# Kernel tuning notes

Hardware: AMD Instinct MI355X
Metric: run time of the kernel (lower is better)

## Reference

```python
import jax, jax.numpy as jnp
import numpy as np

EPS = 1e-05
B, M, N, P = 32, 1024, 1024, 256


def _xavier(key, shape):
    fan_in, fan_out = shape[0], shape[1]
    limit = np.sqrt(6.0 / (fan_in + fan_out))
    return jax.random.uniform(key, shape, jnp.float32, -limit, limit)


def setup_inputs() -> dict:
    key = jax.random.key(0)
    ks = jax.random.split(key, 6)
    return {
        "x": jax.random.normal(ks[0], (B, M, N), jnp.float32),
        "original_xj_y": _xavier(ks[1], (N, P)),
        "original_xi_y": _xavier(ks[2], (M, P)),
        "permuted_xj_y": _xavier(ks[3], (M, P)),
        "permuted_xi_y": _xavier(ks[4], (N, P)),
        "gamma_o_sum": jnp.ones((P,), jnp.float32),
        "gamma_o": jnp.ones((P, P), jnp.float32),
        "gamma_p_sum": jnp.ones((P,), jnp.float32),
        "gamma_p": jnp.ones((P, P), jnp.float32),
        "gamma": jnp.ones((P, P), jnp.float32),
        "beta_o_sum": jnp.zeros((P,), jnp.float32),
        "beta_o": jnp.zeros((P, P), jnp.float32),
        "beta_p_sum": jnp.zeros((P,), jnp.float32),
        "beta_p": jnp.zeros((P, P), jnp.float32),
        "beta": jnp.zeros((P, P), jnp.float32),
    }


def _normalize(x, axes, gamma, beta):
    mean = jnp.mean(x, axis=axes, keepdims=True)
    std = jnp.sqrt(jnp.var(x, axis=axes, keepdims=True, ddof=1))  # torch std is unbiased
    return gamma * ((x - mean) / (std + EPS)) + beta


def reference(x, original_xj_y, original_xi_y, permuted_xj_y, permuted_xi_y,
              gamma_o_sum, gamma_o, gamma_p_sum, gamma_p, gamma,
              beta_o_sum, beta_o, beta_p_sum, beta_p, beta):
    permuted = jnp.swapaxes(x, -1, -2)  # [B, N, M]

    # original path
    oyy = x @ original_xj_y                      # [B, M, P]
    o_sum = _normalize(oyy.sum(axis=-2), (-1,), gamma_o_sum, beta_o_sum) + 1.0  # [B, P]
    oyy = jnp.swapaxes(oyy, -1, -2) @ original_xi_y  # [B, P, P]
    oyy = jnp.swapaxes(oyy, -1, -2)
    oyy = _normalize(oyy, (-2, -1), gamma_o, beta_o)

    # permuted path
    pyy = permuted @ permuted_xj_y               # [B, N, P]
    p_sum = _normalize(pyy.sum(axis=-2), (-1,), gamma_p_sum, beta_p_sum) + 1.0  # [B, P]
    pyy = jnp.swapaxes(pyy, -1, -2) @ permuted_xi_y  # [B, P, P]
    pyy = jnp.swapaxes(pyy, -1, -2)
    pyy = _normalize(pyy, (-2, -1), gamma_p, beta_p)

    relations = jnp.einsum('ij,ik->ijk', o_sum, p_sum)  # [B, P, P]
    projected = (oyy * relations) @ (pyy * relations)   # [B, P, P]
    projected = _normalize(projected, (-2, -1), gamma, beta)
    return (projected, relations)
```

## Files before the change

kernel.cpp:

```cpp
#include <hip/hip_runtime.h>
#include <hip/hip_bf16.h>

#define PP 256
#define BB 32
#define MM 1024
#define NN 1024

constexpr float EPSF = 1e-5f;

typedef __attribute__((ext_vector_type(8))) short short8v;
typedef __attribute__((ext_vector_type(4))) short short4v;
typedef __attribute__((ext_vector_type(4))) float f32x4;

__device__ inline float bf2f(short s) {
  union { unsigned u; float f; } cv;
  cv.u = ((unsigned)(unsigned short)s) << 16;
  return cv.f;
}
__device__ inline short f2bf(float f) {
  union { float f; unsigned u; } cv; cv.f = f;
  unsigned u = cv.u;
  unsigned r = (u + 0x7fffu + ((u >> 16) & 1u)) >> 16;
  return (short)r;
}

__device__ inline void gload16(const void* g, void* l) {
  __builtin_amdgcn_global_load_lds(
      (const __attribute__((address_space(1))) unsigned*)g,
      (__attribute__((address_space(3))) unsigned*)l, 16, 0, 0);
}

__global__ __launch_bounds__(256)
void wconv4(const float* __restrict__ s0, const float* __restrict__ s1,
            const float* __restrict__ s2, const float* __restrict__ s3,
            short* __restrict__ d0, short* __restrict__ d1,
            short* __restrict__ d2, short* __restrict__ d3)
{
  const float* src = (blockIdx.z == 0) ? s0 : (blockIdx.z == 1) ? s1
                    : (blockIdx.z == 2) ? s2 : s3;
  short* dst = (blockIdx.z == 0) ? d0 : (blockIdx.z == 1) ? d1
              : (blockIdx.z == 2) ? d2 : d3;
  __shared__ float tile[64][65];
  const int c0 = blockIdx.x * 64, r0 = blockIdx.y * 64;
  const int tid = threadIdx.x;
#pragma unroll
  for (int i = 0; i < 16; ++i) {
    int idx = i * 256 + tid;
    int r = idx >> 6, c = idx & 63;
    tile[r][c] = src[(long)(r0 + r) * 256 + (c0 + c)];
  }
  __syncthreads();
#pragma unroll
  for (int i = 0; i < 16; ++i) {
    int idx = i * 256 + tid;
    int rr = idx >> 6, cc = idx & 63;
    dst[(long)(c0 + rr) * 1024 + (r0 + cc)] = f2bf(tile[cc][rr]);
  }
}

__global__ __launch_bounds__(256)
void tr2_f32(const float* __restrict__ s0, const float* __restrict__ s1,
             float* __restrict__ d0, float* __restrict__ d1)
{
  const float* src = blockIdx.z ? s1 : s0;
  float* dst = blockIdx.z ? d1 : d0;
  __shared__ float tile[64][65];
  const int c0 = blockIdx.x * 64, r0 = blockIdx.y * 64;
  const int tid = threadIdx.x;
#pragma unroll
  for (int i = 0; i < 16; ++i) {
    int idx = i * 256 + tid;
    int r = idx >> 6, c = idx & 63;
    tile[r][c] = src[(long)(r0 + r) * 256 + (c0 + c)];
  }
  __syncthreads();
#pragma unroll
  for (int i = 0; i < 16; ++i) {
    int idx = i * 256 + tid;
    int rr = idx >> 6, cc = idx & 63;
    dst[(long)(c0 + rr) * 256 + (r0 + cc)] = tile[cc][rr];
  }
}

__global__ __launch_bounds__(256, 4)
void gemm_xcat(const float* __restrict__ x, const short* __restrict__ wcat,
               short* __restrict__ oyyT, short* __restrict__ UT,
               float* __restrict__ rowsum)
{
  constexpr int BM = 128, BN = 128;
  __shared__ short As[2][4 * BM * 8];
  __shared__ short Bs[2][4 * BN * 8];

  const int b = blockIdx.z;
  const float* Ab = x + (long)b * MM * NN;
  const int m0 = blockIdx.x * BM;
  const int n0 = blockIdx.y * BN;

  const int tid = threadIdx.x;
  const int l = tid & 63, w = tid >> 6;
  const int wr = w >> 1, wc = w & 1;
  const int lk = l >> 4, lr = l & 15;
  const int sm = tid >> 2, skc = tid & 3;

  const float* aptr0 = Ab + (long)(m0 + sm) * NN + skc * 8;
  const float* aptr1 = Ab + (long)(m0 + 64 + sm) * NN + skc * 8;
  const int bn = tid & 127, bk0 = (tid >> 7) * 8;
  const short* bptr = wcat + (long)(n0 + bn) * NN + bk0;

  const int sA0 = ((skc * BM + sm) * 8) ^ (skc << 4);
  const int sA1 = ((skc * BM + 64 + sm) * 8) ^ (skc << 4);

  f32x4 acc[4][4];
#pragma unroll
  for (int fm = 0; fm < 4; ++fm)
#pragma unroll
    for (int fn = 0; fn < 4; ++fn)
      acc[fm][fn] = (f32x4){0.f, 0.f, 0.f, 0.f};

  float rs0 = 0.f, rs1 = 0.f;
  const bool doRs = (blockIdx.y == 0);
  float4 a00, a01, a10, a11;

#define XCAT_LOAD_A(k0_) do { \
    a00 = *reinterpret_cast<const float4*>(aptr0 + (k0_)); \
    a01 = *reinterpret_cast<const float4*>(aptr0 + (k0_) + 4); \
    a10 = *reinterpret_cast<const float4*>(aptr1 + (k0_)); \
    a11 = *reinterpret_cast<const float4*>(aptr1 + (k0_) + 4); \
  } while (0)

#define XCAT_STAGE_B(buf_, k0_) do { \
    gload16(bptr + (k0_), &Bs[buf_][tid * 8]); \
    gload16(bptr + (k0_) + 16, &Bs[buf_][(tid + 256) * 8]); \
  } while (0)

#define XCAT_STAGE_A(buf_) do { \
    if (doRs) { \
      rs0 += a00.x + a00.y + a00.z + a00.w + a01.x + a01.y + a01.z + a01.w; \
      rs1 += a10.x + a10.y + a10.z + a10.w + a11.x + a11.y + a11.z + a11.w; \
    } \
    short8v pk0, pk1; \
    pk0[0] = f2bf(a00.x); pk0[1] = f2bf(a00.y); pk0[2] = f2bf(a00.z); pk0[3] = f2bf(a00.w); \
    pk0[4] = f2bf(a01.x); pk0[5] = f2bf(a01.y); pk0[6] = f2bf(a01.z); pk0[7] = f2bf(a01.w); \
    pk1[0] = f2bf(a10.x); pk1[1] = f2bf(a10.y); pk1[2] = f2bf(a10.z); pk1[3] = f2bf(a10.w); \
    pk1[4] = f2bf(a11.x); pk1[5] = f2bf(a11.y); pk1[6] = f2bf(a11.z); pk1[7] = f2bf(a11.w); \
    *reinterpret_cast<short8v*>(&As[buf_][sA0]) = pk0; \
    *reinterpret_cast<short8v*>(&As[buf_][sA1]) = pk1; \
  } while (0)

  XCAT_LOAD_A(0);
  XCAT_STAGE_B(0, 0);
  XCAT_STAGE_A(0);
  __syncthreads();

  for (int kt = 0; kt < 32; ++kt) {
    const int cur = kt & 1, nxt = cur ^ 1;
    if (kt < 31) {
      const int k1 = (kt + 1) * 32;
      XCAT_LOAD_A(k1);
      XCAT_STAGE_B(nxt, k1);
    }
    short8v af[4], bf[4];
#pragma unroll
    for (int fm = 0; fm < 4; ++fm) {
      const int row = wr * 64 + fm * 16 + lr;
      af[fm] = *reinterpret_cast<const short8v*>(&As[cur][((lk * BM + row) * 8) ^ (lk << 4)]);
    }
#pragma unroll
    for (int fn = 0; fn < 4; ++fn)
      bf[fn] = *reinterpret_cast<const short8v*>(&Bs[cur][(lk * BN + wc * 64 + fn * 16 + lr) * 8]);
#pragma unroll
    for (int fm = 0; fm < 4; ++fm)
#pragma unroll
      for (int fn = 0; fn < 4; ++fn)
        acc[fm][fn] = __builtin_amdgcn_mfma_f32_16x16x32_bf16(
            af[fm], bf[fn], acc[fm][fn], 0, 0, 0);
    if (kt < 31) XCAT_STAGE_A(nxt);
    __syncthreads();
  }

  if (doRs) {
    rs0 += __shfl_xor(rs0, 1); rs0 += __shfl_xor(rs0, 2);
    rs1 += __shfl_xor(rs1, 1); rs1 += __shfl_xor(rs1, 2);
    if ((tid & 3) == 0) {
      rowsum[(long)b * MM + m0 + sm] = rs0;
      rowsum[(long)b * MM + m0 + 64 + sm] = rs1;
    }
  }

  short* Cb = ((n0 < 256) ? oyyT : UT) + (long)b * PP * MM;
  const int nb = n0 & 255;
#pragma unroll
  for (int fm = 0; fm < 4; ++fm)
#pragma unroll
    for (int fn = 0; fn < 4; ++fn) {
      const int c = nb + wc * 64 + fn * 16 + lr;
      const int rb = m0 + wr * 64 + fm * 16 + lk * 4;
      short4v pk;
#pragma unroll
      for (int j = 0; j < 4; ++j) pk[j] = f2bf(acc[fm][fn][j]);
      *reinterpret_cast<short4v*>(&Cb[(long)c * MM + rb]) = pk;
    }
}

__global__ __launch_bounds__(256)
void gemm_dual(const short* __restrict__ oyyT, const short* __restrict__ wo2T,
               const short* __restrict__ UT, const short* __restrict__ wp1T,
               float* __restrict__ t2T, float* __restrict__ p2)
{
  constexpr int BM = 64, BN = 64;
  __shared__ short As[2][4 * BM * 8];
  __shared__ short Bs[2][4 * BN * 8];

  const int z = blockIdx.z;
  const short* Ab; const short* Bb; float* Cb;
  if (z < 32) { Ab = oyyT + (long)z * PP * MM; Bb = wo2T; Cb = t2T + ((long)z << 16); }
  else { Ab = UT + (long)(z - 32) * PP * MM; Bb = wp1T; Cb = p2 + ((long)(z - 32) << 16); }

  const int m0 = blockIdx.x * BM, n0 = blockIdx.y * BN;
  const int tid = threadIdx.x;
  const int l = tid & 63, w = tid >> 6;
  const int wr = w >> 1, wc = w & 1;
  const int lk = l >> 4, lr = l & 15;
  const int kc = tid >> 6, mloc = tid & 63;
  const short* aP = Ab + (long)(m0 + mloc) * MM + kc * 8;
  const short* bP = Bb + (long)(n0 + mloc) * MM + kc * 8;

  f32x4 acc[2][2];
#pragma unroll
  for (int fm = 0; fm < 2; ++fm)
#pragma unroll
    for (int fn = 0; fn < 2; ++fn)
      acc[fm][fn] = (f32x4){0.f, 0.f, 0.f, 0.f};

  gload16(aP, &As[0][tid * 8]);
  gload16(bP, &Bs[0][tid * 8]);
  __syncthreads();

  for (int kt = 0; kt < 32; ++kt) {
    const int cur = kt & 1, nxt = cur ^ 1;
    if (kt < 31) {
      gload16(aP + (kt + 1) * 32, &As[nxt][tid * 8]);
      gload16(bP + (kt + 1) * 32, &Bs[nxt][tid * 8]);
    }
    short8v af[2], bf[2];
#pragma unroll
    for (int fm = 0; fm < 2; ++fm)
      af[fm] = *(const short8v*)&As[cur][(lk * BM + wr * 32 + fm * 16 + lr) * 8];
#pragma unroll
    for (int fn = 0; fn < 2; ++fn)
      bf[fn] = *(const short8v*)&Bs[cur][(lk * BN + wc * 32 + fn * 16 + lr) * 8];
#pragma unroll
    for (int fm = 0; fm < 2; ++fm)
#pragma unroll
      for (int fn = 0; fn < 2; ++fn)
        acc[fm][fn] = __builtin_amdgcn_mfma_f32_16x16x32_bf16(
            af[fm], bf[fn], acc[fm][fn], 0, 0, 0);
    __syncthreads();
  }

#pragma unroll
  for (int fm = 0; fm < 2; ++fm)
#pragma unroll
    for (int fn = 0; fn < 2; ++fn) {
      const int c = n0 + wc * 32 + fn * 16 + lr;
      const int rb = m0 + wr * 32 + fm * 16 + lk * 4;
      *(f32x4*)&Cb[(long)c * PP + rb] = acc[fm][fn];
    }
}

__global__ __launch_bounds__(256)
void gemm_pp(const short* __restrict__ A, const short* __restrict__ BT,
             float* __restrict__ C)
{
  constexpr int BM = 64, BN = 64;
  __shared__ short As[2][4 * BM * 8];
  __shared__ short Bs[2][4 * BN * 8];
  const int b = blockIdx.z;
  const short* Ab = A + ((long)b << 16);
  const short* Bb = BT + ((long)b << 16);
  float* Cb = C + ((long)b << 16);
  const int m0 = blockIdx.x * BM, n0 = blockIdx.y * BN;
  const int tid = threadIdx.x;
  const int l = tid & 63, w = tid >> 6;
  const int wr = w >> 1, wc = w & 1;
  const int lk = l >> 4, lr = l & 15;
  const int kc = tid >> 6, mloc = tid & 63;
  const short* aP = Ab + (long)(m0 + mloc) * PP + kc * 8;
  const short* bP = Bb + (long)(n0 + mloc) * PP + kc * 8;

  f32x4 acc[2][2];
#pragma unroll
  for (int fm = 0; fm < 2; ++fm)
#pragma unroll
    for (int fn = 0; fn < 2; ++fn)
      acc[fm][fn] = (f32x4){0.f, 0.f, 0.f, 0.f};

  gload16(aP, &As[0][tid * 8]);
  gload16(bP, &Bs[0][tid * 8]);
  __syncthreads();

  for (int kt = 0; kt < 8; ++kt) {
    const int cur = kt & 1, nxt = cur ^ 1;
    if (kt < 7) {
      gload16(aP + (kt + 1) * 32, &As[nxt][tid * 8]);
      gload16(bP + (kt + 1) * 32, &Bs[nxt][tid * 8]);
    }
    short8v af[2], bf[2];
#pragma unroll
    for (int fm = 0; fm < 2; ++fm)
      af[fm] = *(const short8v*)&As[cur][(lk * BM + wr * 32 + fm * 16 + lr) * 8];
#pragma unroll
    for (int fn = 0; fn < 2; ++fn)
      bf[fn] = *(const short8v*)&Bs[cur][(lk * BN + wc * 32 + fn * 16 + lr) * 8];
#pragma unroll
    for (int fm = 0; fm < 2; ++fm)
#pragma unroll
      for (int fn = 0; fn < 2; ++fn)
        acc[fm][fn] = __builtin_amdgcn_mfma_f32_16x16x32_bf16(
            af[fm], bf[fn], acc[fm][fn], 0, 0, 0);
    __syncthreads();
  }

#pragma unroll
  for (int fm = 0; fm < 2; ++fm)
#pragma unroll
    for (int fn = 0; fn < 2; ++fn) {
      const int c = n0 + wc * 32 + fn * 16 + lr;
      const int rb = m0 + wr * 32 + fm * 16 + lk * 4;
#pragma unroll
      for (int j = 0; j < 4; ++j)
        Cb[(long)(rb + j) * PP + c] = acc[fm][fn][j];
    }
}

__global__ __launch_bounds__(256)
void colsum_bf16(const short* __restrict__ srcT, float* __restrict__ raw)
{
  const int b = blockIdx.y;
  const int w = threadIdx.x >> 6, l = threadIdx.x & 63;
  const int p = blockIdx.x * 4 + w;
  const short* row = srcT + ((long)b * 256 + p) * 1024;
  short8v v1 = *(const short8v*)&row[l * 8];
  short8v v2 = *(const short8v*)&row[(64 + l) * 8];
  float s = 0.f;
#pragma unroll
  for (int j = 0; j < 8; ++j) s += bf2f(v1[j]) + bf2f(v2[j]);
#pragma unroll
  for (int off = 32; off; off >>= 1) s += __shfl_down(s, off);
  if (l == 0) raw[(long)b * 256 + p] = s;
}

__global__ __launch_bounds__(256)
void psum_dot(const short* __restrict__ wp1T, const float* __restrict__ rowsum,
              float* __restrict__ rawP)
{
  __shared__ float rsm[1024];
  const int b = blockIdx.x;
  for (int i = threadIdx.x; i < 1024; i += 256) rsm[i] = rowsum[(long)b * 1024 + i];
  __syncthreads();
  const int p = threadIdx.x;
  const short* wrow = wp1T + (long)p * 1024;
  float s = 0.f;
  for (int k = 0; k < 1024; k += 8) {
    short8v v = *(const short8v*)&wrow[k];
#pragma unroll
    for (int j = 0; j < 8; ++j) s = fmaf(bf2f(v[j]), rsm[k + j], s);
  }
  rawP[(long)b * 256 + p] = s;
}

__device__ inline void block_reduce2(float& v1, float& v2, float* red)
{
#pragma unroll
  for (int off = 32; off > 0; off >>= 1) {
    v1 += __shfl_down(v1, off);
    v2 += __shfl_down(v2, off);
  }
  const int lane = threadIdx.x & 63, wid = threadIdx.x >> 6;
  if (lane == 0) { red[wid * 2] = v1; red[wid * 2 + 1] = v2; }
  __syncthreads();
  v1 = red[0] + red[2] + red[4] + red[6];
  v2 = red[1] + red[3] + red[5] + red[7];
}

__global__ __launch_bounds__(256)
void norm_sum2(const float* __restrict__ raw2,
               const float* __restrict__ g_os, const float* __restrict__ b_os,
               const float* __restrict__ g_ps, const float* __restrict__ b_ps,
               float* __restrict__ o_sum, float* __restrict__ p_sum)
{
  const int bb = blockIdx.x;
  const bool isP = bb >= 32;
  const int b = bb & 31;
  const float* raw = raw2 + (isP ? 8192 : 0);
  const float* gamma = isP ? g_ps : g_os;
  const float* beta = isP ? b_ps : b_os;
  float* outp = isP ? p_sum : o_sum;
  const int p = threadIdx.x;
  float s = raw[(long)b * 256 + p];
  __shared__ float red[8];
  float v1 = s, v2 = s * s;
  block_reduce2(v1, v2, red);
  const float mean = v1 / 256.0f;
  float var = fmaxf((v2 - v1 * mean) / 255.0f, 0.f);
  const float inv = 1.0f / (sqrtf(var) + EPSF);
  outp[(long)b * 256 + p] = gamma[p] * (s - mean) * inv + beta[p] + 1.0f;
}

__global__ __launch_bounds__(256)
void stats_dual(const float* __restrict__ t2T, const float* __restrict__ p2,
                float* __restrict__ part)
{
  const int y = blockIdx.y, chunk = blockIdx.x;
  const float* s = (y < 32 ? t2T + ((long)y << 16)
                           : p2 + ((long)(y - 32) << 16)) + (long)chunk * 8192;
  float v1 = 0.f, v2 = 0.f;
  for (int i = threadIdx.x; i < 2048; i += 256) {
    float4 xv = *reinterpret_cast<const float4*>(&s[i * 4]);
    v1 += xv.x + xv.y + xv.z + xv.w;
    v2 = fmaf(xv.x, xv.x, fmaf(xv.y, xv.y, fmaf(xv.z, xv.z, fmaf(xv.w, xv.w, v2))));
  }
  __shared__ float red[8];
  block_reduce2(v1, v2, red);
  if (threadIdx.x == 0) {
    part[(y * 8 + chunk) * 2] = v1;
    part[(y * 8 + chunk) * 2 + 1] = v2;
  }
}

__global__ void stats_fin2(const float* __restrict__ part,
                           float* __restrict__ stO, float* __restrict__ stP)
{
  const int t = threadIdx.x;
  float v1 = 0.f, v2 = 0.f;
#pragma unroll
  for (int c = 0; c < 8; ++c) {
    v1 += part[(t * 8 + c) * 2];
    v2 += part[(t * 8 + c) * 2 + 1];
  }
  const float mean = v1 / 65536.0f;
  const float var = fmaxf((v2 - v1 * mean) / 65535.0f, 0.f);
  float* st = (t < 32) ? stO : stP;
  st[(t & 31) * 2] = mean;
  st[(t & 31) * 2 + 1] = 1.0f / (sqrtf(var) + EPSF);
}

__global__ __launch_bounds__(256)
void stats_part(const float* __restrict__ src, float* __restrict__ part)
{
  const int b = blockIdx.y, chunk = blockIdx.x;
  const float* s = src + ((long)b << 16) + (long)chunk * 8192;
  float v1 = 0.f, v2 = 0.f;
  for (int i = threadIdx.x; i < 2048; i += 256) {
    float4 xv = *reinterpret_cast<const float4*>(&s[i * 4]);
    v1 += xv.x + xv.y + xv.z + xv.w;
    v2 = fmaf(xv.x, xv.x, fmaf(xv.y, xv.y, fmaf(xv.z, xv.z, fmaf(xv.w, xv.w, v2))));
  }
  __shared__ float red[8];
  block_reduce2(v1, v2, red);
  if (threadIdx.x == 0) {
    part[(b * 8 + chunk) * 2] = v1;
    part[(b * 8 + chunk) * 2 + 1] = v2;
  }
}

__global__ void stats_fin(const float* __restrict__ part, float* __restrict__ st)
{
  const int b = threadIdx.x;
  if (b < 32) {
    float v1 = 0.f, v2 = 0.f;
#pragma unroll
    for (int c = 0; c < 8; ++c) {
      v1 += part[(b * 8 + c) * 2];
      v2 += part[(b * 8 + c) * 2 + 1];
    }
    const float mean = v1 / 65536.0f;
    const float var = fmaxf((v2 - v1 * mean) / 65535.0f, 0.f);
    st[b * 2] = mean;
    st[b * 2 + 1] = 1.0f / (sqrtf(var) + EPSF);
  }
}

__global__ __launch_bounds__(256)
void prep2(const float* __restrict__ t2T, const float* __restrict__ p2,
           const float* __restrict__ o_sum, const float* __restrict__ p_sum,
           const float* __restrict__ gamma_o, const float* __restrict__ beta_o,
           const float* __restrict__ gTp, const float* __restrict__ bTp,
           const float* __restrict__ stO, const float* __restrict__ stP,
           short* __restrict__ Ap, short* __restrict__ BpT,
           float* __restrict__ out)
{
  const long idx = (long)blockIdx.x * 256 + threadIdx.x;
  const int b = (int)(idx >> 16);
  const int rc = (int)(idx & 65535);
  const int r = rc >> 8, c = rc & 255;
  const float mO = stO[b * 2], iO = stO[b * 2 + 1];
  const float mP = stP[b * 2], iP = stP[b * 2 + 1];
  const float relA = o_sum[(b << 8) + r] * p_sum[(b << 8) + c];
  const float on = gamma_o[rc] * (t2T[idx] - mO) * iO + beta_o[rc];
  Ap[idx] = f2bf(on * relA);
  const float pn = gTp[rc] * (p2[idx] - mP) * iP + bTp[rc];
  BpT[idx] = f2bf(pn * o_sum[(b << 8) + c] * p_sum[(b << 8) + r]);
  out[(long)BB * 65536 + idx] = relA;
}

__global__ __launch_bounds__(256)
void final_half(const float* __restrict__ proj, const float* __restrict__ stF,
                const float* __restrict__ gamma, const float* __restrict__ beta,
                float* __restrict__ out)
{
  const long idx = (long)blockIdx.x * 256 + threadIdx.x;
  const int b = (int)(idx >> 16);
  const int ij = (int)(idx & 65535);
  out[idx] = gamma[ij] * (proj[idx] - stF[b * 2]) * stF[b * 2 + 1] + beta[ij];
}

extern "C" void kernel_launch(void* const* d_in, const int* in_sizes, int n_in,
                              void* d_out, int out_size, void* d_ws, size_t ws_size,
                              hipStream_t stream)
{
  const float* x    = (const float*)d_in[0];
  const float* Wo1  = (const float*)d_in[1];
  const float* Wo2  = (const float*)d_in[2];
  const float* Wp1  = (const float*)d_in[3];
  const float* Wp2  = (const float*)d_in[4];
  const float* g_os = (const float*)d_in[5];
  const float* g_o  = (const float*)d_in[6];
  const float* g_ps = (const float*)d_in[7];
  const float* g_p  = (const float*)d_in[8];
  const float* g    = (const float*)d_in[9];
  const float* b_os = (const float*)d_in[10];
  const float* b_o  = (const float*)d_in[11];
  const float* b_ps = (const float*)d_in[12];
  const float* b_p  = (const float*)d_in[13];
  const float* b_   = (const float*)d_in[14];
  float* out = (float*)d_out;

  short* wcat = (short*)d_ws;
  short* wo2T = wcat + 524288;
  short* wp1T = wo2T + 262144;
  short* oyyT = wp1T + 262144;
  short* UT   = oyyT + 8388608;
  float* gTp  = (float*)(UT + 8388608);
  float* bTp  = gTp + 65536;
  float* rowsumX = bTp + 65536;
  float* t2T  = rowsumX + 32768;
  float* p2   = t2T + 2097152;
  float* proj = p2 + 2097152;
  short* Ap   = (short*)(proj + 2097152);
  short* BpT  = Ap + 2097152;
  float* raw2 = (float*)(BpT + 2097152);
  float* o_sum = raw2 + 16384;
  float* p_sum = o_sum + 8192;
  float* part  = p_sum + 8192;
  float* partF = part + 1024;
  float* stO   = partF + 512;
  float* stP   = stO + 64;
  float* stF   = stP + 64;

  wconv4<<<dim3(4, 16, 4), 256, 0, stream>>>(Wo1, Wo2, Wp1, Wp2,
                                             wcat, wo2T, wp1T, wcat + 262144);
  tr2_f32<<<dim3(4, 4, 2), 256, 0, stream>>>(g_p, b_p, gTp, bTp);

  gemm_xcat<<<dim3(8, 4, 32), 256, 0, stream>>>(x, wcat, oyyT, UT, rowsumX);

  colsum_bf16<<<dim3(64, 32), 256, 0, stream>>>(oyyT, raw2);
  psum_dot<<<32, 256, 0, stream>>>(wp1T, rowsumX, raw2 + 8192);
  norm_sum2<<<64, 256, 0, stream>>>(raw2, g_os, b_os, g_ps, b_ps, o_sum, p_sum);

  gemm_dual<<<dim3(4, 4, 64), 256, 0, stream>>>(oyyT, wo2T, UT, wp1T, t2T, p2);

  stats_dual<<<dim3(8, 64), 256, 0, stream>>>(t2T, p2, part);
  stats_fin2<<<1, 64, 0, stream>>>(part, stO, stP);

  prep2<<<8192, 256, 0, stream>>>(t2T, p2, o_sum, p_sum, g_o, b_o, gTp, bTp,
                                  stO, stP, Ap, BpT, out);

  gemm_pp<<<dim3(4, 4, 32), 256, 0, stream>>>(Ap, BpT, proj);

  stats_part<<<dim3(8, 32), 256, 0, stream>>>(proj, partF);
  stats_fin<<<1, 64, 0, stream>>>(partF, stF);

  final_half<<<8192, 256, 0, stream>>>(proj, stF, g, b_, out);
}
```

Measured before the change: 168.9 us.

## Retile x GEMM to full-width 64x512 blocks and enlarge dual GEMM tiles

The first GEMM now uses 512-thread blocks that each cover 64 rows of x against all 512 output columns. Each x tile is therefore read from global memory and converted to bf16 only once, where before it was re-read by four column blocks. Half the threads load and convert A while the other half stage B, so the work is split between warps. The second GEMM grows its tiles from 64x64 to 128x128 for more reuse per block, at the cost of fewer blocks (256) and more registers and LDS per block.

```diff
diff --git a/kernel.cpp b/kernel.cpp
--- a/kernel.cpp
+++ b/kernel.cpp
@@ -82,33 +82,26 @@
   }
 }
 
-__global__ __launch_bounds__(256, 4)
+__global__ __launch_bounds__(512, 4)
 void gemm_xcat(const float* __restrict__ x, const short* __restrict__ wcat,
                short* __restrict__ oyyT, short* __restrict__ UT,
                float* __restrict__ rowsum)
 {
-  constexpr int BM = 128, BN = 128;
-  __shared__ short As[2][4 * BM * 8];
-  __shared__ short Bs[2][4 * BN * 8];
+  __shared__ short As[2][4 * 64 * 8];
+  __shared__ short Bs[2][4 * 512 * 8];
 
   const int b = blockIdx.z;
   const float* Ab = x + (long)b * MM * NN;
-  const int m0 = blockIdx.x * BM;
-  const int n0 = blockIdx.y * BN;
+  const int m0 = blockIdx.x * 64;
 
   const int tid = threadIdx.x;
   const int l = tid & 63, w = tid >> 6;
-  const int wr = w >> 1, wc = w & 1;
   const int lk = l >> 4, lr = l & 15;
-  const int sm = tid >> 2, skc = tid & 3;
-
-  const float* aptr0 = Ab + (long)(m0 + sm) * NN + skc * 8;
-  const float* aptr1 = Ab + (long)(m0 + 64 + sm) * NN + skc * 8;
-  const int bn = tid & 127, bk0 = (tid >> 7) * 8;
-  const short* bptr = wcat + (long)(n0 + bn) * NN + bk0;
-
-  const int sA0 = ((skc * BM + sm) * 8) ^ (skc << 4);
-  const int sA1 = ((skc * BM + 64 + sm) * 8) ^ (skc << 4);
+
+  const int sm = (tid >> 2) & 63, skc = tid & 3;
+  const float* aptr = Ab + (long)(m0 + sm) * NN + skc * 8;
+  const int sA = ((skc * 64 + sm) * 8) ^ (skc << 4);
+  const int t2 = tid & 255;
 
   f32x4 acc[4][4];
 #pragma unroll
@@ -117,84 +110,76 @@
     for (int fn = 0; fn < 4; ++fn)
       acc[fm][fn] = (f32x4){0.f, 0.f, 0.f, 0.f};
 
-  float rs0 = 0.f, rs1 = 0.f;
-  const bool doRs = (blockIdx.y == 0);
-  float4 a00, a01, a10, a11;
-
-#define XCAT_LOAD_A(k0_) do { \
-    a00 = *reinterpret_cast<const float4*>(aptr0 + (k0_)); \
-    a01 = *reinterpret_cast<const float4*>(aptr0 + (k0_) + 4); \
-    a10 = *reinterpret_cast<const float4*>(aptr1 + (k0_)); \
-    a11 = *reinterpret_cast<const float4*>(aptr1 + (k0_) + 4); \
+  float rs = 0.f;
+  float4 a0, a1;
+
+#define XC_LOAD_A(k0_) do { \
+    a0 = *reinterpret_cast<const float4*>(aptr + (k0_)); \
+    a1 = *reinterpret_cast<const float4*>(aptr + (k0_) + 4); \
   } while (0)
 
-#define XCAT_STAGE_B(buf_, k0_) do { \
-    gload16(bptr + (k0_), &Bs[buf_][tid * 8]); \
-    gload16(bptr + (k0_) + 16, &Bs[buf_][(tid + 256) * 8]); \
+#define XC_STAGE_B(buf_, k0_) do { \
+    _Pragma("unroll") \
+    for (int i = 0; i < 8; ++i) { \
+      const int n_ = ((i & 1) << 8) + t2; \
+      const int kc_ = i >> 1; \
+      gload16(wcat + (long)n_ * NN + (k0_) + kc_ * 8, \
+              &Bs[buf_][(kc_ * 512 + n_) * 8]); \
+    } \
   } while (0)
 
-#define XCAT_STAGE_A(buf_) do { \
-    if (doRs) { \
-      rs0 += a00.x + a00.y + a00.z + a00.w + a01.x + a01.y + a01.z + a01.w; \
-      rs1 += a10.x + a10.y + a10.z + a10.w + a11.x + a11.y + a11.z + a11.w; \
-    } \
-    short8v pk0, pk1; \
-    pk0[0] = f2bf(a00.x); pk0[1] = f2bf(a00.y); pk0[2] = f2bf(a00.z); pk0[3] = f2bf(a00.w); \
-    pk0[4] = f2bf(a01.x); pk0[5] = f2bf(a01.y); pk0[6] = f2bf(a01.z); pk0[7] = f2bf(a01.w); \
-    pk1[0] = f2bf(a10.x); pk1[1] = f2bf(a10.y); pk1[2] = f2bf(a10.z); pk1[3] = f2bf(a10.w); \
-    pk1[4] = f2bf(a11.x); pk1[5] = f2bf(a11.y); pk1[6] = f2bf(a11.z); pk1[7] = f2bf(a11.w); \
-    *reinterpret_cast<short8v*>(&As[buf_][sA0]) = pk0; \
-    *reinterpret_cast<short8v*>(&As[buf_][sA1]) = pk1; \
+#define XC_STAGE_A(buf_) do { \
+    rs += a0.x + a0.y + a0.z + a0.w + a1.x + a1.y + a1.z + a1.w; \
+    short8v pk; \
+    pk[0] = f2bf(a0.x); pk[1] = f2bf(a0.y); pk[2] = f2bf(a0.z); pk[3] = f2bf(a0.w); \
+    pk[4] = f2bf(a1.x); pk[5] = f2bf(a1.y); pk[6] = f2bf(a1.z); pk[7] = f2bf(a1.w); \
+    *reinterpret_cast<short8v*>(&As[buf_][sA]) = pk; \
   } while (0)
 
-  XCAT_LOAD_A(0);
-  XCAT_STAGE_B(0, 0);
-  XCAT_STAGE_A(0);
+  if (tid < 256) { XC_LOAD_A(0); XC_STAGE_A(0); }
+  else           { XC_STAGE_B(0, 0); }
   __syncthreads();
 
   for (int kt = 0; kt < 32; ++kt) {
     const int cur = kt & 1, nxt = cur ^ 1;
     if (kt < 31) {
       const int k1 = (kt + 1) * 32;
-      XCAT_LOAD_A(k1);
-      XCAT_STAGE_B(nxt, k1);
+      if (tid < 256) XC_LOAD_A(k1);
+      else           XC_STAGE_B(nxt, k1);
     }
     short8v af[4], bf[4];
 #pragma unroll
-    for (int fm = 0; fm < 4; ++fm) {
-      const int row = wr * 64 + fm * 16 + lr;
-      af[fm] = *reinterpret_cast<const short8v*>(&As[cur][((lk * BM + row) * 8) ^ (lk << 4)]);
-    }
+    for (int fm = 0; fm < 4; ++fm)
+      af[fm] = *reinterpret_cast<const short8v*>(
+          &As[cur][((lk * 64 + fm * 16 + lr) * 8) ^ (lk << 4)]);
 #pragma unroll
     for (int fn = 0; fn < 4; ++fn)
-      bf[fn] = *reinterpret_cast<const short8v*>(&Bs[cur][(lk * BN + wc * 64 + fn * 16 + lr) * 8]);
+      bf[fn] = *reinterpret_cast<const short8v*>(
+          &Bs[cur][(lk * 512 + w * 64 + fn * 16 + lr) * 8]);
 #pragma unroll
     for (int fm = 0; fm < 4; ++fm)
 #pragma unroll
       for (int fn = 0; fn < 4; ++fn)
         acc[fm][fn] = __builtin_amdgcn_mfma_f32_16x16x32_bf16(
             af[fm], bf[fn], acc[fm][fn], 0, 0, 0);
-    if (kt < 31) XCAT_STAGE_A(nxt);
+    if (kt < 31 && tid < 256) XC_STAGE_A(nxt);
     __syncthreads();
   }
 
-  if (doRs) {
-    rs0 += __shfl_xor(rs0, 1); rs0 += __shfl_xor(rs0, 2);
-    rs1 += __shfl_xor(rs1, 1); rs1 += __shfl_xor(rs1, 2);
-    if ((tid & 3) == 0) {
-      rowsum[(long)b * MM + m0 + sm] = rs0;
-      rowsum[(long)b * MM + m0 + 64 + sm] = rs1;
-    }
-  }
-
-  short* Cb = ((n0 < 256) ? oyyT : UT) + (long)b * PP * MM;
-  const int nb = n0 & 255;
+  if (tid < 256) {
+    rs += __shfl_xor(rs, 1);
+    rs += __shfl_xor(rs, 2);
+    if (skc == 0) rowsum[(long)b * MM + m0 + sm] = rs;
+  }
+
+  const int cfull = w * 64;
+  short* Cb = ((cfull < 256) ? oyyT : UT) + (long)b * PP * MM;
 #pragma unroll
   for (int fm = 0; fm < 4; ++fm)
 #pragma unroll
     for (int fn = 0; fn < 4; ++fn) {
-      const int c = nb + wc * 64 + fn * 16 + lr;
-      const int rb = m0 + wr * 64 + fm * 16 + lk * 4;
+      const int c = (cfull & 255) + fn * 16 + lr;
+      const int rb = m0 + fm * 16 + lk * 4;
       short4v pk;
 #pragma unroll
       for (int j = 0; j < 4; ++j) pk[j] = f2bf(acc[fm][fn][j]);
@@ -207,7 +192,7 @@
                const short* __restrict__ UT, const short* __restrict__ wp1T,
                float* __restrict__ t2T, float* __restrict__ p2)
 {
-  constexpr int BM = 64, BN = 64;
+  constexpr int BM = 128, BN = 128;
   __shared__ short As[2][4 * BM * 8];
   __shared__ short Bs[2][4 * BN * 8];
 
@@ -221,49 +206,52 @@
   const int l = tid & 63, w = tid >> 6;
   const int wr = w >> 1, wc = w & 1;
   const int lk = l >> 4, lr = l & 15;
-  const int kc = tid >> 6, mloc = tid & 63;
-  const short* aP = Ab + (long)(m0 + mloc) * MM + kc * 8;
-  const short* bP = Bb + (long)(n0 + mloc) * MM + kc * 8;
-
-  f32x4 acc[2][2];
-#pragma unroll
-  for (int fm = 0; fm < 2; ++fm)
-#pragma unroll
-    for (int fn = 0; fn < 2; ++fn)
+
+  f32x4 acc[4][4];
+#pragma unroll
+  for (int fm = 0; fm < 4; ++fm)
+#pragma unroll
+    for (int fn = 0; fn < 4; ++fn)
       acc[fm][fn] = (f32x4){0.f, 0.f, 0.f, 0.f};
 
-  gload16(aP, &As[0][tid * 8]);
-  gload16(bP, &Bs[0][tid * 8]);
+#define GD_STAGE(buf_, k0_) do { \
+    _Pragma("unroll") \
+    for (int i = 0; i < 2; ++i) { \
+      const int s_ = i * 256 + tid; \
+      const int kc_ = s_ >> 7, mm_ = s_ & 127; \
+      gload16(Ab + (long)(m0 + mm_) * MM + (k0_) + kc_ * 8, &As[buf_][s_ * 8]); \
+      gload16(Bb + (long)(n0 + mm_) * MM + (k0_) + kc_ * 8, &Bs[buf_][s_ * 8]); \
+    } \
+  } while (0)
+
+  GD_STAGE(0, 0);
   __syncthreads();
 
   for (int kt = 0; kt < 32; ++kt) {
     const int cur = kt & 1, nxt = cur ^ 1;
-    if (kt < 31) {
-      gload16(aP + (kt + 1) * 32, &As[nxt][tid * 8]);
-      gload16(bP + (kt + 1) * 32, &Bs[nxt][tid * 8]);
-    }
-    short8v af[2], bf[2];
-#pragma unroll
-    for (int fm = 0; fm < 2; ++fm)
-      af[fm] = *(const short8v*)&As[cur][(lk * BM + wr * 32 + fm * 16 + lr) * 8];
-#pragma unroll
-    for (int fn = 0; fn < 2; ++fn)
-      bf[fn] = *(const short8v*)&Bs[cur][(lk * BN + wc * 32 + fn * 16 + lr) * 8];
-#pragma unroll
-    for (int fm = 0; fm < 2; ++fm)
-#pragma unroll
-      for (int fn = 0; fn < 2; ++fn)
+    if (kt < 31) GD_STAGE(nxt, (kt + 1) * 32);
+    short8v af[4], bf[4];
+#pragma unroll
+    for (int fm = 0; fm < 4; ++fm)
+      af[fm] = *(const short8v*)&As[cur][(lk * BM + wr * 64 + fm * 16 + lr) * 8];
+#pragma unroll
+    for (int fn = 0; fn < 4; ++fn)
+      bf[fn] = *(const short8v*)&Bs[cur][(lk * BN + wc * 64 + fn * 16 + lr) * 8];
+#pragma unroll
+    for (int fm = 0; fm < 4; ++fm)
+#pragma unroll
+      for (int fn = 0; fn < 4; ++fn)
         acc[fm][fn] = __builtin_amdgcn_mfma_f32_16x16x32_bf16(
             af[fm], bf[fn], acc[fm][fn], 0, 0, 0);
     __syncthreads();
   }
 
 #pragma unroll
-  for (int fm = 0; fm < 2; ++fm)
-#pragma unroll
-    for (int fn = 0; fn < 2; ++fn) {
-      const int c = n0 + wc * 32 + fn * 16 + lr;
-      const int rb = m0 + wr * 32 + fm * 16 + lk * 4;
+  for (int fm = 0; fm < 4; ++fm)
+#pragma unroll
+    for (int fn = 0; fn < 4; ++fn) {
+      const int c = n0 + wc * 64 + fn * 16 + lr;
+      const int rb = m0 + wr * 64 + fm * 16 + lk * 4;
       *(f32x4*)&Cb[(long)c * PP + rb] = acc[fm][fn];
     }
 }
@@ -562,13 +550,13 @@
                                              wcat, wo2T, wp1T, wcat + 262144);
   tr2_f32<<<dim3(4, 4, 2), 256, 0, stream>>>(g_p, b_p, gTp, bTp);
 
-  gemm_xcat<<<dim3(8, 4, 32), 256, 0, stream>>>(x, wcat, oyyT, UT, rowsumX);
+  gemm_xcat<<<dim3(16, 1, 32), 512, 0, stream>>>(x, wcat, oyyT, UT, rowsumX);
 
   colsum_bf16<<<dim3(64, 32), 256, 0, stream>>>(oyyT, raw2);
   psum_dot<<<32, 256, 0, stream>>>(wp1T, rowsumX, raw2 + 8192);
   norm_sum2<<<64, 256, 0, stream>>>(raw2, g_os, b_os, g_ps, b_ps, o_sum, p_sum);
 
-  gemm_dual<<<dim3(4, 4, 64), 256, 0, stream>>>(oyyT, wo2T, UT, wp1T, t2T, p2);
+  gemm_dual<<<dim3(2, 2, 64), 256, 0, stream>>>(oyyT, wo2T, UT, wp1T, t2T, p2);
 
   stats_dual<<<dim3(8, 64), 256, 0, stream>>>(t2T, p2, part);
   stats_fin2<<<1, 64, 0, stream>>>(part, stO, stP);
```

New measurement: 253.6 us. +50.1%, slower.

## Stage fp32 x directly to LDS via async loads and split sums into separate kernel

Applied to the files above, without the earlier changes.

The main GEMM now copies fp32 x tiles straight into shared memory with global_load_lds and converts them to bf16 at fragment-read time using packed cvt instructions. Before, each thread loaded x into registers, converted it and stored it to LDS. Row sums are removed from the GEMM. A new sums_x kernel rereads x to compute row and column sums, and msum_norm computes o_sum and p_sum from those sums and the weights, replacing colsum_bf16, psum_dot and norm_sum2. This cuts register pressure and the conversion work on the GEMM's critical path, but doubles the LDS footprint for A, adds a full extra pass over x, and changes o_sum numerics (fp32 column sums instead of a sum over bf16 oyy).

```diff
diff --git a/kernel.cpp b/kernel.cpp
--- a/kernel.cpp
+++ b/kernel.cpp
@@ -22,6 +22,15 @@
   unsigned u = cv.u;
   unsigned r = (u + 0x7fffu + ((u >> 16) & 1u)) >> 16;
   return (short)r;
+}
+
+__device__ inline short8v cvt8(f32x4 lo, f32x4 hi) {
+  union { int i[4]; short8v s; } u;
+  asm("v_cvt_pk_bf16_f32 %0, %1, %2" : "=v"(u.i[0]) : "v"(lo[0]), "v"(lo[1]));
+  asm("v_cvt_pk_bf16_f32 %0, %1, %2" : "=v"(u.i[1]) : "v"(lo[2]), "v"(lo[3]));
+  asm("v_cvt_pk_bf16_f32 %0, %1, %2" : "=v"(u.i[2]) : "v"(hi[0]), "v"(hi[1]));
+  asm("v_cvt_pk_bf16_f32 %0, %1, %2" : "=v"(u.i[3]) : "v"(hi[2]), "v"(hi[3]));
+  return u.s;
 }
 
 __device__ inline void gload16(const void* g, void* l) {
@@ -82,33 +91,22 @@
   }
 }
 
-__global__ __launch_bounds__(256, 4)
+__global__ __launch_bounds__(256)
 void gemm_xcat(const float* __restrict__ x, const short* __restrict__ wcat,
-               short* __restrict__ oyyT, short* __restrict__ UT,
-               float* __restrict__ rowsum)
-{
-  constexpr int BM = 128, BN = 128;
-  __shared__ short As[2][4 * BM * 8];
-  __shared__ short Bs[2][4 * BN * 8];
+               short* __restrict__ oyyT, short* __restrict__ UT)
+{
+  __shared__ float Asf[2][4096];
+  __shared__ short Bs[2][4096];
 
   const int b = blockIdx.z;
   const float* Ab = x + (long)b * MM * NN;
-  const int m0 = blockIdx.x * BM;
-  const int n0 = blockIdx.y * BN;
+  const int m0 = blockIdx.x * 128;
+  const int n0 = blockIdx.y * 128;
 
   const int tid = threadIdx.x;
   const int l = tid & 63, w = tid >> 6;
   const int wr = w >> 1, wc = w & 1;
   const int lk = l >> 4, lr = l & 15;
-  const int sm = tid >> 2, skc = tid & 3;
-
-  const float* aptr0 = Ab + (long)(m0 + sm) * NN + skc * 8;
-  const float* aptr1 = Ab + (long)(m0 + 64 + sm) * NN + skc * 8;
-  const int bn = tid & 127, bk0 = (tid >> 7) * 8;
-  const short* bptr = wcat + (long)(n0 + bn) * NN + bk0;
-
-  const int sA0 = ((skc * BM + sm) * 8) ^ (skc << 4);
-  const int sA1 = ((skc * BM + 64 + sm) * 8) ^ (skc << 4);
 
   f32x4 acc[4][4];
 #pragma unroll
@@ -117,74 +115,47 @@
     for (int fn = 0; fn < 4; ++fn)
       acc[fm][fn] = (f32x4){0.f, 0.f, 0.f, 0.f};
 
-  float rs0 = 0.f, rs1 = 0.f;
-  const bool doRs = (blockIdx.y == 0);
-  float4 a00, a01, a10, a11;
-
-#define XCAT_LOAD_A(k0_) do { \
-    a00 = *reinterpret_cast<const float4*>(aptr0 + (k0_)); \
-    a01 = *reinterpret_cast<const float4*>(aptr0 + (k0_) + 4); \
-    a10 = *reinterpret_cast<const float4*>(aptr1 + (k0_)); \
-    a11 = *reinterpret_cast<const float4*>(aptr1 + (k0_) + 4); \
+#define XC_STAGE(buf_, k0_) do { \
+    _Pragma("unroll") \
+    for (int i = 0; i < 4; ++i) { \
+      const int s_ = i * 256 + tid; \
+      const int kc_ = s_ >> 7, m_ = s_ & 127; \
+      gload16(Ab + (long)(m0 + m_) * NN + (k0_) + kc_ * 4, &Asf[buf_][s_ * 4]); \
+    } \
+    _Pragma("unroll") \
+    for (int i = 0; i < 2; ++i) { \
+      const int s_ = i * 256 + tid; \
+      const int kc_ = s_ >> 7, n_ = s_ & 127; \
+      gload16(wcat + (long)(n0 + n_) * NN + (k0_) + kc_ * 8, &Bs[buf_][s_ * 8]); \
+    } \
   } while (0)
 
-#define XCAT_STAGE_B(buf_, k0_) do { \
-    gload16(bptr + (k0_), &Bs[buf_][tid * 8]); \
-    gload16(bptr + (k0_) + 16, &Bs[buf_][(tid + 256) * 8]); \
-  } while (0)
-
-#define XCAT_STAGE_A(buf_) do { \
-    if (doRs) { \
-      rs0 += a00.x + a00.y + a00.z + a00.w + a01.x + a01.y + a01.z + a01.w; \
-      rs1 += a10.x + a10.y + a10.z + a10.w + a11.x + a11.y + a11.z + a11.w; \
-    } \
-    short8v pk0, pk1; \
-    pk0[0] = f2bf(a00.x); pk0[1] = f2bf(a00.y); pk0[2] = f2bf(a00.z); pk0[3] = f2bf(a00.w); \
-    pk0[4] = f2bf(a01.x); pk0[5] = f2bf(a01.y); pk0[6] = f2bf(a01.z); pk0[7] = f2bf(a01.w); \
-    pk1[0] = f2bf(a10.x); pk1[1] = f2bf(a10.y); pk1[2] = f2bf(a10.z); pk1[3] = f2bf(a10.w); \
-    pk1[4] = f2bf(a11.x); pk1[5] = f2bf(a11.y); pk1[6] = f2bf(a11.z); pk1[7] = f2bf(a11.w); \
-    *reinterpret_cast<short8v*>(&As[buf_][sA0]) = pk0; \
-    *reinterpret_cast<short8v*>(&As[buf_][sA1]) = pk1; \
-  } while (0)
-
-  XCAT_LOAD_A(0);
-  XCAT_STAGE_B(0, 0);
-  XCAT_STAGE_A(0);
+  XC_STAGE(0, 0);
   __syncthreads();
 
   for (int kt = 0; kt < 32; ++kt) {
     const int cur = kt & 1, nxt = cur ^ 1;
-    if (kt < 31) {
-      const int k1 = (kt + 1) * 32;
-      XCAT_LOAD_A(k1);
-      XCAT_STAGE_B(nxt, k1);
-    }
+    if (kt < 31) XC_STAGE(nxt, (kt + 1) * 32);
+
     short8v af[4], bf[4];
 #pragma unroll
     for (int fm = 0; fm < 4; ++fm) {
       const int row = wr * 64 + fm * 16 + lr;
-      af[fm] = *reinterpret_cast<const short8v*>(&As[cur][((lk * BM + row) * 8) ^ (lk << 4)]);
+      f32x4 lo = *reinterpret_cast<const f32x4*>(&Asf[cur][((2 * lk) * 128 + row) * 4]);
+      f32x4 hi = *reinterpret_cast<const f32x4*>(&Asf[cur][((2 * lk + 1) * 128 + row) * 4]);
+      af[fm] = cvt8(lo, hi);
     }
 #pragma unroll
     for (int fn = 0; fn < 4; ++fn)
-      bf[fn] = *reinterpret_cast<const short8v*>(&Bs[cur][(lk * BN + wc * 64 + fn * 16 + lr) * 8]);
+      bf[fn] = *reinterpret_cast<const short8v*>(
+          &Bs[cur][(lk * 128 + wc * 64 + fn * 16 + lr) * 8]);
 #pragma unroll
     for (int fm = 0; fm < 4; ++fm)
 #pragma unroll
       for (int fn = 0; fn < 4; ++fn)
         acc[fm][fn] = __builtin_amdgcn_mfma_f32_16x16x32_bf16(
             af[fm], bf[fn], acc[fm][fn], 0, 0, 0);
-    if (kt < 31) XCAT_STAGE_A(nxt);
     __syncthreads();
-  }
-
-  if (doRs) {
-    rs0 += __shfl_xor(rs0, 1); rs0 += __shfl_xor(rs0, 2);
-    rs1 += __shfl_xor(rs1, 1); rs1 += __shfl_xor(rs1, 2);
-    if ((tid & 3) == 0) {
-      rowsum[(long)b * MM + m0 + sm] = rs0;
-      rowsum[(long)b * MM + m0 + 64 + sm] = rs1;
-    }
   }
 
   short* Cb = ((n0 < 256) ? oyyT : UT) + (long)b * PP * MM;
@@ -200,6 +171,104 @@
       for (int j = 0; j < 4; ++j) pk[j] = f2bf(acc[fm][fn][j]);
       *reinterpret_cast<short4v*>(&Cb[(long)c * MM + rb]) = pk;
     }
+}
+
+__global__ __launch_bounds__(256)
+void sums_x(const float* __restrict__ x, float* __restrict__ colpart,
+            float* __restrict__ rowsumX)
+{
+  __shared__ float rw[64][4];
+  const int stripe = blockIdx.x, b = blockIdx.y;
+  const int t = threadIdx.x;
+  const int wv = t >> 6, ln = t & 63;
+  const float* base = x + ((long)b * MM + stripe * 64) * NN + 4 * t;
+  float4 colacc = make_float4(0.f, 0.f, 0.f, 0.f);
+  for (int r = 0; r < 64; ++r) {
+    float4 v = *reinterpret_cast<const float4*>(base + (long)r * NN);
+    colacc.x += v.x; colacc.y += v.y; colacc.z += v.z; colacc.w += v.w;
+    float rp = v.x + v.y + v.z + v.w;
+#pragma unroll
+    for (int off = 32; off; off >>= 1) rp += __shfl_xor(rp, off);
+    if (ln == 0) rw[r][wv] = rp;
+  }
+  *reinterpret_cast<float4*>(&colpart[((long)b * 16 + stripe) * 1024 + 4 * t]) = colacc;
+  __syncthreads();
+  if (t < 64)
+    rowsumX[(long)b * MM + stripe * 64 + t] = rw[t][0] + rw[t][1] + rw[t][2] + rw[t][3];
+}
+
+__global__ __launch_bounds__(256)
+void msum_norm(const float* __restrict__ colpart, const float* __restrict__ rowsumX,
+               const short* __restrict__ wcat, const short* __restrict__ wp1T,
+               const float* __restrict__ g_os, const float* __restrict__ b_os,
+               const float* __restrict__ g_ps, const float* __restrict__ b_ps,
+               float* __restrict__ o_sum, float* __restrict__ p_sum)
+{
+  __shared__ float cs[1024];
+  __shared__ float rs[1024];
+  __shared__ float red[8];
+  const int b = blockIdx.x;
+  const int t = threadIdx.x;
+#pragma unroll
+  for (int i = 0; i < 4; ++i) {
+    const int col = i * 256 + t;
+    float s = 0.f;
+#pragma unroll
+    for (int st = 0; st < 16; ++st)
+      s += colpart[((long)b * 16 + st) * 1024 + col];
+    cs[col] = s;
+    rs[col] = rowsumX[(long)b * 1024 + col];
+  }
+  __syncthreads();
+
+  const short* worow = wcat + (long)t * 1024;
+  const short* wprow = wp1T + (long)t * 1024;
+  float oraw = 0.f, praw = 0.f;
+  for (int k = 0; k < 1024; k += 8) {
+    short8v wo = *(const short8v*)&worow[k];
+    short8v wp = *(const short8v*)&wprow[k];
+#pragma unroll
+    for (int j = 0; j < 8; ++j) {
+      oraw = fmaf(bf2f(wo[j]), cs[k + j], oraw);
+      praw = fmaf(bf2f(wp[j]), rs[k + j], praw);
+    }
+  }
+
+  {
+    float v1 = oraw, v2 = oraw * oraw;
+#pragma unroll
+    for (int off = 32; off > 0; off >>= 1) {
+      v1 += __shfl_down(v1, off);
+      v2 += __shfl_down(v2, off);
+    }
+    const int lane = t & 63, wid = t >> 6;
+    if (lane == 0) { red[wid * 2] = v1; red[wid * 2 + 1] = v2; }
+    __syncthreads();
+    v1 = red[0] + red[2] + red[4] + red[6];
+    v2 = red[1] + red[3] + red[5] + red[7];
+    const float mean = v1 / 256.0f;
+    const float var = fmaxf((v2 - v1 * mean) / 255.0f, 0.f);
+    const float inv = 1.0f / (sqrtf(var) + EPSF);
+    o_sum[(long)b * 256 + t] = g_os[t] * (oraw - mean) * inv + b_os[t] + 1.0f;
+  }
+  __syncthreads();
+  {
+    float v1 = praw, v2 = praw * praw;
+#pragma unroll
+    for (int off = 32; off > 0; off >>= 1) {
+      v1 += __shfl_down(v1, off);
+      v2 += __shfl_down(v2, off);
+    }
+    const int lane = t & 63, wid = t >> 6;
+    if (lane == 0) { red[wid * 2] = v1; red[wid * 2 + 1] = v2; }
+    __syncthreads();
+    v1 = red[0] + red[2] + red[4] + red[6];
+    v2 = red[1] + red[3] + red[5] + red[7];
+    const float mean = v1 / 256.0f;
+    const float var = fmaxf((v2 - v1 * mean) / 255.0f, 0.f);
+    const float inv = 1.0f / (sqrtf(var) + EPSF);
+    p_sum[(long)b * 256 + t] = g_ps[t] * (praw - mean) * inv + b_ps[t] + 1.0f;
+  }
 }
 
 __global__ __launch_bounds__(256)
@@ -333,42 +402,6 @@
     }
 }
 
-__global__ __launch_bounds__(256)
-void colsum_bf16(const short* __restrict__ srcT, float* __restrict__ raw)
-{
-  const int b = blockIdx.y;
-  const int w = threadIdx.x >> 6, l = threadIdx.x & 63;
-  const int p = blockIdx.x * 4 + w;
-  const short* row = srcT + ((long)b * 256 + p) * 1024;
-  short8v v1 = *(const short8v*)&row[l * 8];
-  short8v v2 = *(const short8v*)&row[(64 + l) * 8];
-  float s = 0.f;
-#pragma unroll
-  for (int j = 0; j < 8; ++j) s += bf2f(v1[j]) + bf2f(v2[j]);
-#pragma unroll
-  for (int off = 32; off; off >>= 1) s += __shfl_down(s, off);
-  if (l == 0) raw[(long)b * 256 + p] = s;
-}
-
-__global__ __launch_bounds__(256)
-void psum_dot(const short* __restrict__ wp1T, const float* __restrict__ rowsum,
-              float* __restrict__ rawP)
-{
-  __shared__ float rsm[1024];
-  const int b = blockIdx.x;
-  for (int i = threadIdx.x; i < 1024; i += 256) rsm[i] = rowsum[(long)b * 1024 + i];
-  __syncthreads();
-  const int p = threadIdx.x;
-  const short* wrow = wp1T + (long)p * 1024;
-  float s = 0.f;
-  for (int k = 0; k < 1024; k += 8) {
-    short8v v = *(const short8v*)&wrow[k];
-#pragma unroll
-    for (int j = 0; j < 8; ++j) s = fmaf(bf2f(v[j]), rsm[k + j], s);
-  }
-  rawP[(long)b * 256 + p] = s;
-}
-
 __device__ inline void block_reduce2(float& v1, float& v2, float* red)
 {
 #pragma unroll
@@ -381,30 +414,6 @@
   __syncthreads();
   v1 = red[0] + red[2] + red[4] + red[6];
   v2 = red[1] + red[3] + red[5] + red[7];
-}
-
-__global__ __launch_bounds__(256)
-void norm_sum2(const float* __restrict__ raw2,
-               const float* __restrict__ g_os, const float* __restrict__ b_os,
-               const float* __restrict__ g_ps, const float* __restrict__ b_ps,
-               float* __restrict__ o_sum, float* __restrict__ p_sum)
-{
-  const int bb = blockIdx.x;
-  const bool isP = bb >= 32;
-  const int b = bb & 31;
-  const float* raw = raw2 + (isP ? 8192 : 0);
-  const float* gamma = isP ? g_ps : g_os;
-  const float* beta = isP ? b_ps : b_os;
-  float* outp = isP ? p_sum : o_sum;
-  const int p = threadIdx.x;
-  float s = raw[(long)b * 256 + p];
-  __shared__ float red[8];
-  float v1 = s, v2 = s * s;
-  block_reduce2(v1, v2, red);
-  const float mean = v1 / 256.0f;
-  float var = fmaxf((v2 - v1 * mean) / 255.0f, 0.f);
-  const float inv = 1.0f / (sqrtf(var) + EPSF);
-  outp[(long)b * 256 + p] = gamma[p] * (s - mean) * inv + beta[p] + 1.0f;
 }
 
 __global__ __launch_bounds__(256)
@@ -544,13 +553,13 @@
   float* gTp  = (float*)(UT + 8388608);
   float* bTp  = gTp + 65536;
   float* rowsumX = bTp + 65536;
-  float* t2T  = rowsumX + 32768;
+  float* colpart = rowsumX + 32768;
+  float* t2T  = colpart + 524288;
   float* p2   = t2T + 2097152;
   float* proj = p2 + 2097152;
   short* Ap   = (short*)(proj + 2097152);
   short* BpT  = Ap + 2097152;
-  float* raw2 = (float*)(BpT + 2097152);
-  float* o_sum = raw2 + 16384;
+  float* o_sum = (float*)(BpT + 2097152);
   float* p_sum = o_sum + 8192;
   float* part  = p_sum + 8192;
   float* partF = part + 1024;
@@ -562,11 +571,11 @@
                                              wcat, wo2T, wp1T, wcat + 262144);
   tr2_f32<<<dim3(4, 4, 2), 256, 0, stream>>>(g_p, b_p, gTp, bTp);
 
-  gemm_xcat<<<dim3(8, 4, 32), 256, 0, stream>>>(x, wcat, oyyT, UT, rowsumX);
-
-  colsum_bf16<<<dim3(64, 32), 256, 0, stream>>>(oyyT, raw2);
-  psum_dot<<<32, 256, 0, stream>>>(wp1T, rowsumX, raw2 + 8192);
-  norm_sum2<<<64, 256, 0, stream>>>(raw2, g_os, b_os, g_ps, b_ps, o_sum, p_sum);
+  gemm_xcat<<<dim3(8, 4, 32), 256, 0, stream>>>(x, wcat, oyyT, UT);
+
+  sums_x<<<dim3(16, 32), 256, 0, stream>>>(x, colpart, rowsumX);
+  msum_norm<<<32, 256, 0, stream>>>(colpart, rowsumX, wcat, wp1T,
+                                    g_os, b_os, g_ps, b_ps, o_sum, p_sum);
 
   gemm_dual<<<dim3(4, 4, 64), 256, 0, stream>>>(oyyT, wo2T, UT, wp1T, t2T, p2);
 
```

Result: slower. 258.7 us (+53.1%).
